# Kernel tuning notes

Measured on AMD Instinct MI355X. Metric: run time of the kernel, lower is better.

Reference implementation:

```python
import jax, jax.numpy as jnp
import numpy as np

B, T, D = 8, 512, 512
MAX_DUR = 15          # durations drawn from [0,16) then clamped to >=1
MAX_LEN = T * MAX_DUR # static padded frame length (torch pads to per-batch max)


def setup_inputs() -> dict:
    key = jax.random.key(0)
    kf, kd = jax.random.split(key)
    features = jax.random.normal(kf, (B, T, D), dtype=jnp.float32)
    durations = jax.random.randint(kd, (B, T), 0, 16, dtype=jnp.int32)
    return {"features": features, "durations": durations}


def reference(features, durations):
    """Duration-based length regulation (variable-length expand + pad).

    For each batch b, phoneme t is repeated durations[b,t] times along the
    frame axis; sequences are zero-padded to MAX_LEN. Implemented as a
    vectorized cumsum + searchsorted gather (no per-element host syncs).
    """
    Bv, Tv, Dv = features.shape
    dur = jnp.maximum(durations, 1)               # clamp(min=1) as in forward()
    cum = jnp.cumsum(dur, axis=1)                 # (B, T) exclusive-right frame boundaries
    pos = jnp.arange(MAX_LEN, dtype=cum.dtype)    # (MAX_LEN,)
    # idx[b, n] = source phoneme for output frame n: count of boundaries <= n
    idx = jax.vmap(lambda c: jnp.searchsorted(c, pos, side="right"))(cum)  # (B, MAX_LEN)
    valid = pos[None, :] < cum[:, -1:]            # (B, MAX_LEN) frames within total length
    idx = jnp.minimum(idx, Tv - 1)                # keep gather in-bounds for padded frames
    out = jnp.take_along_axis(features, idx[..., None], axis=1)  # (B, MAX_LEN, D)
    return jnp.where(valid[..., None], out, jnp.zeros((), features.dtype))
```

## Files before the change

### kernel.cpp

```cpp
#include <hip/hip_runtime.h>

#define BB 8
#define TT 512
#define DD 512
#define MAX_LEN 7680
#define FPB 60
#define HPB (FPB / 2)
#define BPB (MAX_LEN / FPB)

__global__ __launch_bounds__(256) void regulate_kernel(
    const float4* __restrict__ feat,
    const int*    __restrict__ dur,
    float4*       __restrict__ out)
{
    __shared__ int idx_s[FPB];

    const int t    = threadIdx.x;
    const int b    = blockIdx.x / BPB;
    const int base = (blockIdx.x % BPB) * FPB;
    const int lim  = base + FPB;

    if (t < 64) {
        const int l = t;
        const int4* d4 = (const int4*)(dur + b * TT + 8 * l);
        int4 a = d4[0], c = d4[1];
        int d[8] = {a.x, a.y, a.z, a.w, c.x, c.y, c.z, c.w};
        int s[8];
        int run = 0;
#pragma unroll
        for (int i = 0; i < 8; ++i) {
            int di = d[i] < 1 ? 1 : d[i];
            run += di;
            s[i] = run;
        }
        int incl = run;
#pragma unroll
        for (int off = 1; off < 64; off <<= 1) {
            int v = __shfl_up(incl, off, 64);
            if (l >= off) incl += v;
        }
        const int pre = incl - run;

        for (int j = l; j < FPB; j += 64) idx_s[j] = -1;
#pragma unroll
        for (int i = 0; i < 8; ++i) {
            int st = pre + (i ? s[i - 1] : 0);
            int en = pre + s[i];
            st = st > base ? st : base;
            en = en < lim ? en : lim;
            for (int k = st; k < en; ++k) idx_s[k - base] = 8 * l + i;
        }
    }
    __syncthreads();

    const int lane = t & 127;
    const int sub  = t >> 7;
    const int off  = sub * HPB;
    const float4* featb = feat + (size_t)b * TT * (DD / 4) + lane;
    float4*       outb  = out  + ((size_t)b * MAX_LEN + base + off) * (DD / 4) + lane;

    int    prev = -2;
    float4 val  = make_float4(0.f, 0.f, 0.f, 0.f);
#pragma unroll
    for (int j = 0; j < HPB; ++j) {
        const int src = idx_s[off + j];
        if (src != prev) {
            val = (src >= 0) ? featb[(size_t)src * (DD / 4)]
                             : make_float4(0.f, 0.f, 0.f, 0.f);
            prev = src;
        }
        outb[(size_t)j * (DD / 4)] = val;
    }
}

extern "C" void kernel_launch(void* const* d_in, const int* in_sizes, int n_in,
                              void* d_out, int out_size, void* d_ws, size_t ws_size,
                              hipStream_t stream) {
    const float* feat;
    const int*   dur;
    if (in_sizes[0] == BB * TT) {
        dur  = (const int*)d_in[0];
        feat = (const float*)d_in[1];
    } else {
        feat = (const float*)d_in[0];
        dur  = (const int*)d_in[1];
    }
    float* out = (float*)d_out;

    regulate_kernel<<<BB * BPB, 256, 0, stream>>>(
        (const float4*)feat, dur, (float4*)out);
}
```

Measured before the change: 141.0 us.

## Parallelize over source phonemes with scatter writes and split zero padding

Replaces the frame-major gather, in which each block builds a frame-to-phoneme index table in shared memory, with a phoneme-major scatter. Each block owns four phonemes, loads their feature rows once and writes them repeatedly to their output frame ranges. The zero padding after the total length is split evenly across blocks. This removes the shared-memory table, the __syncthreads and the repeated source loads, but the store work per block now varies with the durations, so the load can be unbalanced across blocks.

```diff
diff --git a/kernel.cpp b/kernel.cpp
--- a/kernel.cpp
+++ b/kernel.cpp
@@ -4,73 +4,83 @@
 #define TT 512
 #define DD 512
 #define MAX_LEN 7680
-#define FPB 60
-#define HPB (FPB / 2)
-#define BPB (MAX_LEN / FPB)
+#define PPB 4
+#define BPB (TT / PPB)
 
 __global__ __launch_bounds__(256) void regulate_kernel(
     const float4* __restrict__ feat,
     const int*    __restrict__ dur,
     float4*       __restrict__ out)
 {
-    __shared__ int idx_s[FPB];
-
     const int t    = threadIdx.x;
-    const int b    = blockIdx.x / BPB;
-    const int base = (blockIdx.x % BPB) * FPB;
-    const int lim  = base + FPB;
-
-    if (t < 64) {
-        const int l = t;
-        const int4* d4 = (const int4*)(dur + b * TT + 8 * l);
-        int4 a = d4[0], c = d4[1];
-        int d[8] = {a.x, a.y, a.z, a.w, c.x, c.y, c.z, c.w};
-        int s[8];
-        int run = 0;
-#pragma unroll
-        for (int i = 0; i < 8; ++i) {
-            int di = d[i] < 1 ? 1 : d[i];
-            run += di;
-            s[i] = run;
-        }
-        int incl = run;
-#pragma unroll
-        for (int off = 1; off < 64; off <<= 1) {
-            int v = __shfl_up(incl, off, 64);
-            if (l >= off) incl += v;
-        }
-        const int pre = incl - run;
-
-        for (int j = l; j < FPB; j += 64) idx_s[j] = -1;
-#pragma unroll
-        for (int i = 0; i < 8; ++i) {
-            int st = pre + (i ? s[i - 1] : 0);
-            int en = pre + s[i];
-            st = st > base ? st : base;
-            en = en < lim ? en : lim;
-            for (int k = st; k < en; ++k) idx_s[k - base] = 8 * l + i;
-        }
-    }
-    __syncthreads();
-
+    const int blk  = blockIdx.x & (BPB - 1);
+    const int b    = blockIdx.x >> 7;
     const int lane = t & 127;
     const int sub  = t >> 7;
-    const int off  = sub * HPB;
+    const int l    = t & 63;
+
+    const int4* d4p = (const int4*)(dur + b * TT + 8 * l);
+    int4 da = d4p[0];
+    int4 db = d4p[1];
+
+    const int ph_a = PPB * blk + 2 * sub;
     const float4* featb = feat + (size_t)b * TT * (DD / 4) + lane;
-    float4*       outb  = out  + ((size_t)b * MAX_LEN + base + off) * (DD / 4) + lane;
+    float4 va = featb[(size_t)ph_a * (DD / 4)];
+    float4 vb = featb[(size_t)(ph_a + 1) * (DD / 4)];
 
-    int    prev = -2;
-    float4 val  = make_float4(0.f, 0.f, 0.f, 0.f);
+    int d[8] = {da.x, da.y, da.z, da.w, db.x, db.y, db.z, db.w};
+    int s[8];
+    int run = 0;
 #pragma unroll
-    for (int j = 0; j < HPB; ++j) {
-        const int src = idx_s[off + j];
-        if (src != prev) {
-            val = (src >= 0) ? featb[(size_t)src * (DD / 4)]
-                             : make_float4(0.f, 0.f, 0.f, 0.f);
-            prev = src;
-        }
-        outb[(size_t)j * (DD / 4)] = val;
+    for (int i = 0; i < 8; ++i) {
+        int di = d[i] < 1 ? 1 : d[i];
+        run += di;
+        s[i] = run;
     }
+    int incl = run;
+#pragma unroll
+    for (int off = 1; off < 64; off <<= 1) {
+        int v = __shfl_up(incl, off, 64);
+        if (l >= off) incl += v;
+    }
+    const int pre = incl - run;
+
+    const int L = blk >> 1;
+    int sm1, sa0, sa1, sa2, sa3;
+    if (blk & 1) {
+        sm1 = __shfl(s[3], L, 64);
+        sa0 = __shfl(s[4], L, 64); sa1 = __shfl(s[5], L, 64);
+        sa2 = __shfl(s[6], L, 64); sa3 = __shfl(s[7], L, 64);
+    } else {
+        sm1 = 0;
+        sa0 = __shfl(s[0], L, 64); sa1 = __shfl(s[1], L, 64);
+        sa2 = __shfl(s[2], L, 64); sa3 = __shfl(s[3], L, 64);
+    }
+    const int preL  = __shfl(pre, L, 64);
+    const int total = __shfl(incl, 63, 64);
+
+    const int st0 = preL + sm1;
+    const int d0 = sa0 - sm1, d1 = sa1 - sa0, d2 = sa2 - sa1, d3 = sa3 - sa2;
+
+    int start, na, nb;
+    if (sub == 0) { start = st0;           na = d0; nb = d1; }
+    else          { start = st0 + d0 + d1; na = d2; nb = d3; }
+
+    float4* outb = out + (size_t)b * MAX_LEN * (DD / 4) + lane;
+    size_t p = (size_t)start * (DD / 4);
+    for (int k = 0; k < na; ++k) { outb[p] = va; p += DD / 4; }
+    for (int k = 0; k < nb; ++k) { outb[p] = vb; p += DD / 4; }
+
+    const int pad = MAX_LEN - total;
+    const int q0  = total + ((pad * blk) >> 7);
+    const int q1  = total + ((pad * (blk + 1)) >> 7);
+    const int h   = q1 - q0;
+    const int mid = q0 + ((h + 1) >> 1);
+    const int z0  = sub == 0 ? q0 : mid;
+    const int z1  = sub == 0 ? mid : q1;
+    const float4 zero = make_float4(0.f, 0.f, 0.f, 0.f);
+    p = (size_t)z0 * (DD / 4);
+    for (int k = z0; k < z1; ++k) { outb[p] = zero; p += DD / 4; }
 }
 
 extern "C" void kernel_launch(void* const* d_in, const int* in_sizes, int n_in,
```

After: 130.5 us (median of 2 runs). -7.4%, faster.
